# Kernel tuning notes

Hardware: AMD Instinct MI355X
Metric: run time of the kernel (lower is better)

## Reference

```python
import jax, jax.numpy as jnp
import numpy as np

B, N, D = 8, 1024, 1024
H, HD = 16, 64          # n_heads, head_dim = D // H
FF = 2 * D              # SwiGLU hidden dim (ffn_dim_mult=2)
EPS = 1e-5


def setup_inputs() -> dict:
    key = jax.random.key(0)
    ks = jax.random.split(key, 10)
    s = 0.02
    return {
        "x": jax.random.normal(ks[0], (B, N, D), dtype=jnp.float32),
        "attn_norm_scale": jnp.ones((D,), jnp.float32),
        "ffn_norm_scale": jnp.ones((D,), jnp.float32),
        "wq": jax.random.normal(ks[1], (D, D), jnp.float32) * s,
        "bq": jnp.zeros((D,), jnp.float32),
        "wk": jax.random.normal(ks[2], (D, D), jnp.float32) * s,
        "bk": jnp.zeros((D,), jnp.float32),
        "wv": jax.random.normal(ks[3], (D, D), jnp.float32) * s,
        "bv": jnp.zeros((D,), jnp.float32),
        "wo": jax.random.normal(ks[4], (D, D), jnp.float32) * s,
        "bo": jnp.zeros((D,), jnp.float32),
        "w_uv": jax.random.normal(ks[5], (D, 2 * FF), jnp.float32) * s,
        "w_out": jax.random.normal(ks[6], (FF, D), jnp.float32) * s,
    }


def _rmsnorm(x, scale):
    xf = x.astype(jnp.float32)
    y = xf * jax.lax.rsqrt(jnp.mean(xf * xf, axis=-1, keepdims=True) + EPS)
    return scale * y.astype(x.dtype)


def reference(x, attn_norm_scale, ffn_norm_scale, wq, bq, wk, bk, wv, bv,
              wo, bo, w_uv, w_out):
    # FFT2D: fft over channel dim then token dim, keep real part
    x = jnp.fft.fft(jnp.fft.fft(x, axis=-1), axis=-2).real.astype(jnp.float32)

    # --- self attention with pre-RMSNorm and residual ---
    xn = _rmsnorm(x, attn_norm_scale)
    q = (xn @ wq + bq).reshape(B, N, H, HD)
    k = (xn @ wk + bk).reshape(B, N, H, HD)
    v = (xn @ wv + bv).reshape(B, N, H, HD)
    scores = jnp.einsum('bnhd,bmhd->bhnm', q, k) / np.sqrt(HD).astype(np.float32)
    attn = jax.nn.softmax(scores, axis=-1)
    o = jnp.einsum('bhnm,bmhd->bnhd', attn, v).reshape(B, N, D)
    x = (o @ wo + bo) + x

    # --- SwiGLU FFN with pre-RMSNorm and residual ---
    xn = _rmsnorm(x, ffn_norm_scale)
    uv = xn @ w_uv                      # [B, N, 2*FF]
    u, vg = uv[..., :FF], uv[..., FF:]
    x = (jax.nn.silu(u) * vg) @ w_out + x
    return x
```

## Files before the change

kernel.cpp:

```cpp
#include <hip/hip_runtime.h>
#include <stdint.h>

typedef unsigned short u16;
typedef __attribute__((ext_vector_type(8))) __bf16 bf16x8;
typedef __attribute__((ext_vector_type(4))) float f32x4;
typedef __attribute__((ext_vector_type(8))) u16 u16x8;

static __device__ __forceinline__ u16 f2bf(float f){
  uint32_t x = __builtin_bit_cast(uint32_t, f);
  x = (x + 0x7FFFu + ((x >> 16) & 1u)) >> 16;
  return (u16)x;
}
static __device__ __forceinline__ u16 f2bf_fast(float f){
  uint32_t x = __builtin_bit_cast(uint32_t, f);
  return (u16)((x + 0x8000u) >> 16);
}
static __device__ __forceinline__ float bf2f(u16 h){
  uint32_t x = ((uint32_t)h) << 16;
  return __builtin_bit_cast(float, x);
}
static __device__ __forceinline__ f32x4 mfma16(bf16x8 a, bf16x8 b, f32x4 c){
  return __builtin_amdgcn_mfma_f32_16x16x32_bf16(a, b, c, 0, 0, 0);
}
static __device__ __forceinline__ void gload16(const void* g, void* l){
  __builtin_amdgcn_global_load_lds(
      (const __attribute__((address_space(1))) void*)(uintptr_t)g,
      (__attribute__((address_space(3))) void*)(uint32_t)(uintptr_t)l,
      16, 0, 0);
}

__global__ __launch_bounds__(256) void k_prep(
    const float* __restrict__ x,  const float* __restrict__ wq,
    const float* __restrict__ wk, const float* __restrict__ wv,
    const float* __restrict__ wo, const float* __restrict__ wuv,
    const float* __restrict__ wout,
    const float* __restrict__ bq, const float* __restrict__ bk,
    const float* __restrict__ bv,
    u16* __restrict__ Cb, u16* __restrict__ Sb, u16* __restrict__ xbt,
    u16* __restrict__ wqkvt, u16* __restrict__ wot, u16* __restrict__ wuvt,
    u16* __restrict__ woutt, float* __restrict__ bqkv)
{
  int bid = blockIdx.x;
  int t = threadIdx.x;
  if (bid < 1024){
    int n = bid, m0 = t * 4;
    #pragma unroll
    for (int i = 0; i < 4; ++i){
      int m = m0 + i;
      int ph = (n * m) & 1023;
      float a = (float)ph * (1.0f / 512.0f);
      int idx = n * 1024 + m;
      Cb[idx] = f2bf(cospif(a)); Sb[idx] = f2bf(sinpif(a));
    }
    return;
  }
  bid -= 1024;
  if (bid >= 18432){
    int i = (bid - 18432) * 256 + t;
    bqkv[i] = i < 1024 ? bq[i] : (i < 2048 ? bk[i - 1024] : bv[i - 2048]);
    return;
  }
  __shared__ float tl[32][33];
  const float* in; u16* out; int Cc, R, bx, by;
  int64_t inOff = 0, outOff = 0;
  bool uvperm = false;
  if (bid < 8192){
    int z = bid >> 10, tile = bid & 1023;
    in = x; out = xbt; Cc = 1024; R = 1024;
    inOff = (int64_t)z << 20; outOff = (int64_t)z << 20;
    bx = tile & 31; by = tile >> 5;
  } else if (bid < 12288){
    int j = (bid - 8192) >> 10, tile = (bid - 8192) & 1023;
    const float* srcs[4] = {wq, wk, wv, wo};
    in = srcs[j]; Cc = 1024; R = 1024;
    if (j < 3){ out = wqkvt; outOff = (int64_t)j << 20; }
    else      { out = wot; }
    bx = tile & 31; by = tile >> 5;
  } else if (bid < 16384){
    int tile = bid - 12288;
    in = wuv; out = wuvt; Cc = 4096; R = 1024; uvperm = true;
    bx = tile & 127; by = tile >> 7;
  } else {
    int tile = bid - 16384;
    in = wout; out = woutt; Cc = 1024; R = 2048;
    bx = tile & 31; by = tile >> 5;
  }
  int tc = bx * 32, tr = by * 32;
  int lx = t & 31, ly = t >> 5;
  const float* ip = in + inOff;
  #pragma unroll
  for (int i = 0; i < 32; i += 8)
    tl[ly + i][lx] = ip[(int64_t)(tr + ly + i) * Cc + tc + lx];
  __syncthreads();
  if (uvperm){
    #pragma unroll
    for (int i = 0; i < 32; i += 8){
      int c = tc + ly + i;
      int pr = (c < 2048) ? ((c >> 4) * 32 + (c & 15))
                          : (((c - 2048) >> 4) * 32 + 16 + ((c - 2048) & 15));
      out[(int64_t)pr * 1024 + tr + lx] = f2bf(tl[lx][ly + i]);
    }
  } else {
    u16* op = out + outOff;
    #pragma unroll
    for (int i = 0; i < 32; i += 8)
      op[(int64_t)(tc + ly + i) * R + tr + lx] = f2bf(tl[lx][ly + i]);
  }
}

__global__ __launch_bounds__(256) void k_rmsnorm(const float* __restrict__ x,
                                                 const float* __restrict__ sc,
                                                 u16* __restrict__ out){
  int r = blockIdx.x;
  const float4* px = (const float4*)(x + (int64_t)r * 1024);
  float4 v = px[threadIdx.x];
  float ss = v.x*v.x + v.y*v.y + v.z*v.z + v.w*v.w;
  #pragma unroll
  for (int o = 1; o < 64; o <<= 1) ss += __shfl_xor(ss, o);
  __shared__ float red[4];
  if ((threadIdx.x & 63) == 0) red[threadIdx.x >> 6] = ss;
  __syncthreads();
  float tot = red[0] + red[1] + red[2] + red[3];
  float rs = rsqrtf(tot * (1.0f / 1024.0f) + 1e-5f);
  float4 s4 = ((const float4*)sc)[threadIdx.x];
  ushort4 ov;
  ov.x = f2bf(v.x * rs * s4.x); ov.y = f2bf(v.y * rs * s4.y);
  ov.z = f2bf(v.z * rs * s4.z); ov.w = f2bf(v.w * rs * s4.w);
  ((ushort4*)(out + (int64_t)r * 1024))[threadIdx.x] = ov;
}

__global__ __launch_bounds__(256) void k_fftfin(const u16* __restrict__ Uw,
                                                const float* __restrict__ sc,
                                                float* __restrict__ Y,
                                                u16* __restrict__ xn){
  int row = blockIdx.x;
  int b = row >> 10, k = row & 1023;
  int kp = (k <= 512) ? k : 1024 - k;
  float sm = (k <= 512) ? 1.0f : -1.0f;
  const u16* ub = Uw + (int64_t)b * 819200 + (int64_t)kp * 640;
  const u16* wb = ub + 640 * 640;
  int c0 = threadIdx.x * 4;
  float y[4];
  #pragma unroll
  for (int i = 0; i < 4; ++i){
    int c = c0 + i;
    int tp = (c <= 512) ? c : 1024 - c;
    float st = (c <= 512) ? sm : -sm;
    y[i] = bf2f(ub[tp]) - st * bf2f(wb[tp]);
  }
  float ss = y[0]*y[0] + y[1]*y[1] + y[2]*y[2] + y[3]*y[3];
  #pragma unroll
  for (int o = 1; o < 64; o <<= 1) ss += __shfl_xor(ss, o);
  __shared__ float red[4];
  if ((threadIdx.x & 63) == 0) red[threadIdx.x >> 6] = ss;
  __syncthreads();
  float tot = red[0] + red[1] + red[2] + red[3];
  float rs = rsqrtf(tot * (1.0f / 1024.0f) + 1e-5f);
  float4 s4 = ((const float4*)sc)[threadIdx.x];
  float4 yo; yo.x = y[0]; yo.y = y[1]; yo.z = y[2]; yo.w = y[3];
  ((float4*)(Y + (int64_t)row * 1024))[threadIdx.x] = yo;
  ushort4 ov;
  ov.x = f2bf(y[0] * rs * s4.x); ov.y = f2bf(y[1] * rs * s4.y);
  ov.z = f2bf(y[2] * rs * s4.z); ov.w = f2bf(y[3] * rs * s4.w);
  ((ushort4*)(xn + (int64_t)row * 1024))[threadIdx.x] = ov;
}

template<bool SILU, bool COLCHUNK>
__global__ __launch_bounds__(256, 4) void k_gemm4(
    const u16* __restrict__ A0, const u16* __restrict__ A1,
    const u16* __restrict__ B0, const u16* __restrict__ B1,
    void* Cout, const float* __restrict__ bias, const float* resid,
    int nkt, int rowSplit, int lda, int ldb, int ldc,
    int64_t aB, int64_t bB, int64_t cB, int outBf16)
{
  __shared__ char smem[32768];

  int z = blockIdx.z;
  int nwg = gridDim.x * gridDim.y;
  int bid = blockIdx.y * gridDim.x + blockIdx.x;
  int q = nwg >> 3, r = nwg & 7, xc = bid & 7, off = bid >> 3;
  int sw = (xc < r ? xc * (q + 1) : r * (q + 1) + (xc - r) * q) + off;
  int bx, by;
  if (COLCHUNK){ bx = sw / gridDim.y; by = sw % gridDim.y; }
  else         { bx = sw % gridDim.x; by = sw / gridDim.x; }

  int tm = by * 128, tn = bx * 128;
  int tid = threadIdx.x;
  int lane = tid & 63, w = tid >> 6;
  int lr = lane & 15, lg = lane >> 4;
  int wOffM = (w >> 1) * 64, wOffN = (w & 1) * 64;

  const u16* Ap = ((tm < rowSplit) ? A0 : A1) + (int64_t)z * aB;
  const u16* Bp = ((tm < rowSplit) ? B0 : B1) + (int64_t)z * bB;
  int64_t cOff = (int64_t)z * cB;

  int r0_, kg0_, r1_, kg1_;
  {
    int D = tid * 16, line = D >> 7, sp = ((D >> 4) & 7) ^ (line & 7);
    r0_ = line * 2 + (sp >> 2); kg0_ = sp & 3;
    D = tid * 16 + 4096; line = D >> 7; sp = ((D >> 4) & 7) ^ (line & 7);
    r1_ = line * 2 + (sp >> 2); kg1_ = sp & 3;
  }
  const u16* pA0 = Ap + (int64_t)(tm + r0_) * lda + kg0_ * 8;
  const u16* pA1 = Ap + (int64_t)(tm + r1_) * lda + kg1_ * 8;
  const u16* pB0 = Bp + (int64_t)(tn + r0_) * ldb + kg0_ * 8;
  const u16* pB1 = Bp + (int64_t)(tn + r1_) * ldb + kg1_ * 8;

  int slotR = (lg + ((lr & 1) << 2)) ^ ((lr >> 1) & 7);
  int aRB = ((wOffM >> 1) + (lr >> 1)) * 128 + slotR * 16;
  int bRB = ((wOffN >> 1) + (lr >> 1)) * 128 + slotR * 16;

  const f32x4 fz = {0.f, 0.f, 0.f, 0.f};
  f32x4 acc[4][4];
  #pragma unroll
  for (int i = 0; i < 4; ++i)
    #pragma unroll
    for (int j = 0; j < 4; ++j) acc[i][j] = fz;

  auto STAGE = [&](int kt, int bf){
    int k0 = kt * 32;
    char* d = smem + bf * 16384 + tid * 16;
    gload16(pA0 + k0, d);
    gload16(pA1 + k0, d + 4096);
    gload16(pB0 + k0, d + 8192);
    gload16(pB1 + k0, d + 12288);
  };
  auto COMPUTE = [&](const char* Ab){
    const char* Bb = Ab + 8192;
    bf16x8 af[4], bfr[4];
    #pragma unroll
    for (int i = 0; i < 4; ++i) af[i]  = *(const bf16x8*)(Ab + aRB + i * 1024);
    #pragma unroll
    for (int j = 0; j < 4; ++j) bfr[j] = *(const bf16x8*)(Bb + bRB + j * 1024);
    #pragma unroll
    for (int i = 0; i < 4; ++i)
      #pragma unroll
      for (int j = 0; j < 4; ++j)
        acc[i][j] = mfma16(af[i], bfr[j], acc[i][j]);
  };

  STAGE(0, 0);
  __syncthreads();
  for (int kt = 0; kt < nkt; kt += 2){
    STAGE(kt + 1, 1);
    COMPUTE(smem);
    __syncthreads();
    if (kt + 2 < nkt) STAGE(kt + 2, 0);
    COMPUTE(smem + 16384);
    __syncthreads();
  }

  if constexpr (SILU){
    int colBase = ((tn + wOffN) >> 1) + lr;
    #pragma unroll
    for (int i = 0; i < 4; ++i){
      #pragma unroll
      for (int jj = 0; jj < 4; ++jj){
        int row = tm + wOffM + i * 16 + lg * 4 + jj;
        #pragma unroll
        for (int jp = 0; jp < 2; ++jp){
          float u = acc[i][jp * 2][jj], v = acc[i][jp * 2 + 1][jj];
          float s = u / (1.0f + __expf(-u));
          ((u16*)Cout)[(int64_t)row * ldc + colBase + jp * 16] = f2bf(s * v);
        }
      }
    }
  } else {
    #pragma unroll
    for (int i = 0; i < 4; ++i){
      #pragma unroll
      for (int j = 0; j < 4; ++j){
        int col = tn + wOffN + j * 16 + lr;
        float badd = bias ? bias[col] : 0.0f;
        #pragma unroll
        for (int jj = 0; jj < 4; ++jj){
          int row = tm + wOffM + i * 16 + lg * 4 + jj;
          int64_t idx = cOff + (int64_t)row * ldc + col;
          float v = acc[i][j][jj] + badd;
          if (resid) v += resid[idx];
          if (outBf16) ((u16*)Cout)[idx] = f2bf(v);
          else         ((float*)Cout)[idx] = v;
        }
      }
    }
  }
}

__global__ __launch_bounds__(256) void k_vtrans(const u16* __restrict__ qkv,
                                                u16* __restrict__ vt){
  __shared__ u16 T[64 * 65];
  int bh = blockIdx.y; int b = bh >> 4, h = bh & 15;
  int kt = blockIdx.x;
  int t = threadIdx.x;
  const u16* src = qkv + (int64_t)(b * 1024 + kt * 64) * 3072 + 2048 + h * 64;
  #pragma unroll
  for (int i = 0; i < 16; ++i){
    int idx = i * 256 + t;
    int r = idx >> 6, c = idx & 63;
    T[r * 65 + c] = src[(int64_t)r * 3072 + c];
  }
  __syncthreads();
  u16* dst = vt + (int64_t)bh * 65536 + kt * 64;
  #pragma unroll
  for (int i = 0; i < 16; ++i){
    int idx = i * 256 + t;
    int dr = idx >> 6, kc = idx & 63;
    dst[(int64_t)dr * 1024 + kc] = T[kc * 65 + dr];
  }
}

__global__ __launch_bounds__(512, 4) void k_attn2(const u16* __restrict__ qkv,
                                                  const u16* __restrict__ vt,
                                                  u16* __restrict__ O){
  __shared__ u16 Ks[2][4096];
  __shared__ u16 Vts[2][4096];
  __shared__ u16 Pl[8][2304];
  int bh = blockIdx.y; int b = bh >> 4, h = bh & 15;
  int qt = blockIdx.x;
  int t = threadIdx.x, w = t >> 6, lane = t & 63, lr = lane & 15, lg = lane >> 4;
  int sr = t >> 3, sl = t & 7;
  int swz = (sl ^ (sr & 7)) * 8;

  const u16* kg = qkv + (int64_t)b * 1024 * 3072 + 1024 + h * 64;
  const u16* vg = vt + (int64_t)bh * 65536;

  const u16* qrow = qkv + (int64_t)(b * 1024 + qt * 256 + w * 32 + lr) * 3072 + h * 64;
  bf16x8 aq[2][2];
  #pragma unroll
  for (int m = 0; m < 2; ++m)
    #pragma unroll
    for (int kc = 0; kc < 2; ++kc)
      aq[m][kc] = *(const bf16x8*)(qrow + (int64_t)m * 16 * 3072 + kc * 32 + lg * 8);

  const f32x4 fz = {0.f, 0.f, 0.f, 0.f};
  f32x4 o_[2][4];
  float lj[2][4];
  #pragma unroll
  for (int m = 0; m < 2; ++m){
    #pragma unroll
    for (int d = 0; d < 4; ++d) o_[m][d] = fz;
    #pragma unroll
    for (int j = 0; j < 4; ++j) lj[m][j] = 0.f;
  }

  #define STAGE(ktile, bn) do {                                                   \
    gload16(kg + (int64_t)((ktile) * 64 + sr) * 3072 + swz,                       \
            (char*)Ks + (bn) * 8192 + t * 16);                                    \
    gload16(vg + (int64_t)sr * 1024 + (ktile) * 64 + swz,                         \
            (char*)Vts + (bn) * 8192 + t * 16);                                   \
  } while (0)

  STAGE(0, 0);
  __syncthreads();
  int buf = 0;
  int lsw = lr & 7;

  const float CSC = 0.1803368801111204f;
  const float MSH = 8.656170245333781f;

  #pragma unroll 1
  for (int kt = 0; kt < 16; ++kt){
    if (kt < 15) STAGE(kt + 1, buf ^ 1);

    f32x4 s[2][4];
    #pragma unroll
    for (int m = 0; m < 2; ++m)
      #pragma unroll
      for (int n = 0; n < 4; ++n) s[m][n] = fz;
    #pragma unroll
    for (int n = 0; n < 4; ++n){
      #pragma unroll
      for (int kc = 0; kc < 2; ++kc){
        bf16x8 kb = *(const bf16x8*)&Ks[buf][(n * 16 + lr) * 64 + (((kc * 4 + lg) ^ lsw) * 8)];
        s[0][n] = mfma16(aq[0][kc], kb, s[0][n]);
        s[1][n] = mfma16(aq[1][kc], kb, s[1][n]);
      }
    }

    #pragma unroll
    for (int m = 0; m < 2; ++m){
      #pragma unroll
      for (int j = 0; j < 4; ++j){
        float p0 = exp2f(fmaf(s[m][0][j], CSC, -MSH));
        float p1 = exp2f(fmaf(s[m][1][j], CSC, -MSH));
        float p2 = exp2f(fmaf(s[m][2][j], CSC, -MSH));
        float p3 = exp2f(fmaf(s[m][3][j], CSC, -MSH));
        lj[m][j] += (p0 + p1) + (p2 + p3);
        u16* pb = &Pl[w][(m * 16 + lg * 4 + j) * 72 + lr];
        pb[0]  = f2bf_fast(p0); pb[16] = f2bf_fast(p1);
        pb[32] = f2bf_fast(p2); pb[48] = f2bf_fast(p3);
      }
    }
    asm volatile("s_waitcnt lgkmcnt(0)" ::: "memory");
    __builtin_amdgcn_sched_barrier(0);

    #pragma unroll
    for (int kc = 0; kc < 2; ++kc){
      bf16x8 pa0 = *(const bf16x8*)&Pl[w][(lr) * 72 + kc * 32 + lg * 8];
      bf16x8 pa1 = *(const bf16x8*)&Pl[w][(16 + lr) * 72 + kc * 32 + lg * 8];
      #pragma unroll
      for (int dt = 0; dt < 4; ++dt){
        bf16x8 vb = *(const bf16x8*)&Vts[buf][(dt * 16 + lr) * 64 + (((kc * 4 + lg) ^ lsw) * 8)];
        o_[0][dt] = mfma16(pa0, vb, o_[0][dt]);
        o_[1][dt] = mfma16(pa1, vb, o_[1][dt]);
      }
    }
    __syncthreads();
    buf ^= 1;
  }
  #undef STAGE

  u16* obase = O + (int64_t)(b * 1024 + qt * 256 + w * 32) * 1024 + h * 64;
  #pragma unroll
  for (int m = 0; m < 2; ++m){
    #pragma unroll
    for (int j = 0; j < 4; ++j){
      float l = lj[m][j];
      l += __shfl_xor(l, 1); l += __shfl_xor(l, 2);
      l += __shfl_xor(l, 4); l += __shfl_xor(l, 8);
      float inv = 1.0f / l;
      int q = m * 16 + lg * 4 + j;
      #pragma unroll
      for (int dt = 0; dt < 4; ++dt)
        obase[(int64_t)q * 1024 + dt * 16 + lr] = f2bf(o_[m][dt][j] * inv);
    }
  }
}

extern "C" void kernel_launch(void* const* d_in, const int* in_sizes, int n_in,
                              void* d_out, int out_size, void* d_ws, size_t ws_size,
                              hipStream_t stream)
{
  (void)in_sizes; (void)n_in; (void)out_size; (void)ws_size;
  const float* x    = (const float*)d_in[0];
  const float* ans  = (const float*)d_in[1];
  const float* fns  = (const float*)d_in[2];
  const float* wq   = (const float*)d_in[3];
  const float* bq   = (const float*)d_in[4];
  const float* wk   = (const float*)d_in[5];
  const float* bk   = (const float*)d_in[6];
  const float* wv   = (const float*)d_in[7];
  const float* bvv  = (const float*)d_in[8];
  const float* wo   = (const float*)d_in[9];
  const float* bo   = (const float*)d_in[10];
  const float* wuv  = (const float*)d_in[11];
  const float* wout = (const float*)d_in[12];

  char* ws = (char*)d_ws;
  const size_t MB = 1u << 20;
  const int64_t M1 = 1024 * 1024;
  const int64_t FB = (int64_t)1280 * 1024;
  const int64_t FB2 = (int64_t)1280 * 640;
  const int BIG = 1 << 30;
  u16*  xbt   = (u16*)(ws + 0 * MB);
  u16*  Xcs   = (u16*)(ws + 16 * MB);
  u16*  Uw    = (u16*)(ws + 36 * MB);
  u16*  xn    = (u16*)(ws + 56 * MB);
  u16*  qkv   = (u16*)(ws + 0 * MB);
  u16*  vtg   = (u16*)(ws + 72 * MB);
  u16*  Obuf  = (u16*)(ws + 88 * MB);
  u16*  xn2   = (u16*)(ws + 0 * MB);
  u16*  g     = (u16*)(ws + 16 * MB);
  u16*  Cb    = (u16*)(ws + 104 * MB);
  u16*  Sb    = (u16*)(ws + 106 * MB);
  u16*  wqkvt = (u16*)(ws + 108 * MB);
  u16*  wot   = (u16*)(ws + 114 * MB);
  u16*  wuvt  = (u16*)(ws + 116 * MB);
  u16*  woutt = (u16*)(ws + 124 * MB);
  float* bqkv = (float*)(ws + 128 * MB);
  float* outF = (float*)d_out;

  k_prep<<<dim3(19468), 256, 0, stream>>>(x, wq, wk, wv, wo, wuv, wout,
      bq, bk, bvv, Cb, Sb, xbt, wqkvt, wot, wuvt, woutt, bqkv);

  k_gemm4<false, true><<<dim3(8, 10, 8), 256, 0, stream>>>(
      Cb, Sb - 640 * 1024, xbt, xbt, Xcs, nullptr, nullptr,
      32, 640, 1024, 1024, 1024, 0, M1, FB, 1);
  k_gemm4<false, false><<<dim3(5, 10, 8), 256, 0, stream>>>(
      Xcs, Xcs, Cb, Sb, Uw, nullptr, nullptr,
      32, 640, 1024, 1024, 640, FB, 0, FB2, 1);
  k_fftfin<<<dim3(8192), 256, 0, stream>>>(Uw, ans, outF, xn);

  k_gemm4<false, false><<<dim3(24, 64, 1), 256, 0, stream>>>(
      xn, xn, wqkvt, wqkvt, qkv, bqkv, nullptr,
      32, BIG, 1024, 1024, 3072, 0, 0, 0, 1);
  k_vtrans<<<dim3(16, 128), 256, 0, stream>>>(qkv, vtg);
  k_attn2<<<dim3(4, 128), 512, 0, stream>>>(qkv, vtg, Obuf);
  k_gemm4<false, false><<<dim3(8, 64, 1), 256, 0, stream>>>(
      Obuf, Obuf, wot, wot, d_out, bo, outF,
      32, BIG, 1024, 1024, 1024, 0, 0, 0, 0);

  k_rmsnorm<<<dim3(8192), 256, 0, stream>>>(outF, fns, xn2);
  k_gemm4<true, false><<<dim3(32, 64, 1), 256, 0, stream>>>(
      xn2, xn2, wuvt, wuvt, g, nullptr, nullptr,
      32, BIG, 1024, 1024, 2048, 0, 0, 0, 1);
  k_gemm4<false, false><<<dim3(8, 64, 1), 256, 0, stream>>>(
      g, g, woutt, woutt, d_out, nullptr, outF,
      64, BIG, 2048, 2048, 1024, 0, 0, 0, 0);
}
```

Measured before the change: 411.4 us.

## Fuse V transpose into QKV GEMM epilogue and group tile rasterization

The QKV projection GEMM now writes the V columns directly in transposed per-head layout into the vt buffer, which removes the separate k_vtrans kernel and its extra global read and write of V. The non-column-chunk GEMMs also switch to a grouped tile ordering of width 16 or 8 columns to improve L2 reuse of the B operand. In exchange, the V part of the QKV output is no longer written to the row-major qkv buffer, and the transposed stores are strided across rows of 1024.

```diff
diff --git a/kernel.cpp b/kernel.cpp
--- a/kernel.cpp
+++ b/kernel.cpp
@@ -170,6 +170,7 @@
     const u16* __restrict__ A0, const u16* __restrict__ A1,
     const u16* __restrict__ B0, const u16* __restrict__ B1,
     void* Cout, const float* __restrict__ bias, const float* resid,
+    u16* __restrict__ vtbuf, int vtn0,
     int nkt, int rowSplit, int lda, int ldb, int ldc,
     int64_t aB, int64_t bB, int64_t cB, int outBf16)
 {
@@ -181,8 +182,16 @@
   int q = nwg >> 3, r = nwg & 7, xc = bid & 7, off = bid >> 3;
   int sw = (xc < r ? xc * (q + 1) : r * (q + 1) + (xc - r) * q) + off;
   int bx, by;
-  if (COLCHUNK){ bx = sw / gridDim.y; by = sw % gridDim.y; }
-  else         { bx = sw % gridDim.x; by = sw / gridDim.x; }
+  if (COLCHUNK){
+    bx = sw / gridDim.y; by = sw % gridDim.y;
+  } else {
+    int gx = gridDim.x;
+    int GW = ((gx & 15) == 0) ? 16 : (((gx & 7) == 0) ? 8 : gx);
+    int gsz = GW * gridDim.y;
+    int grp = sw / gsz, rem = sw % gsz;
+    bx = grp * GW + rem % GW;
+    by = rem / GW;
+  }
 
   int tm = by * 128, tn = bx * 128;
   int tid = threadIdx.x;
@@ -265,47 +274,45 @@
         }
       }
     }
-  } else {
-    #pragma unroll
-    for (int i = 0; i < 4; ++i){
-      #pragma unroll
-      for (int j = 0; j < 4; ++j){
-        int col = tn + wOffN + j * 16 + lr;
-        float badd = bias ? bias[col] : 0.0f;
-        #pragma unroll
-        for (int jj = 0; jj < 4; ++jj){
-          int row = tm + wOffM + i * 16 + lg * 4 + jj;
-          int64_t idx = cOff + (int64_t)row * ldc + col;
-          float v = acc[i][j][jj] + badd;
-          if (resid) v += resid[idx];
-          if (outBf16) ((u16*)Cout)[idx] = f2bf(v);
-          else         ((float*)Cout)[idx] = v;
-        }
+    return;
+  }
+  if (vtbuf && tn >= vtn0){
+    int b = tm >> 10;
+    int key0 = (tm & 1023) + wOffM + lg * 4;
+    #pragma unroll
+    for (int j = 0; j < 4; ++j){
+      int col = tn + wOffN + j * 16 + lr;
+      int hv = (col - 2048) >> 6, d = (col - 2048) & 63;
+      float badd = bias ? bias[col] : 0.0f;
+      u16* vb = vtbuf + ((int64_t)(b * 16 + hv) << 16) + d * 1024;
+      #pragma unroll
+      for (int i = 0; i < 4; ++i){
+        ushort4 pk;
+        pk.x = f2bf(acc[i][j][0] + badd);
+        pk.y = f2bf(acc[i][j][1] + badd);
+        pk.z = f2bf(acc[i][j][2] + badd);
+        pk.w = f2bf(acc[i][j][3] + badd);
+        *(ushort4*)(vb + key0 + i * 16) = pk;
       }
     }
-  }
-}
-
-__global__ __launch_bounds__(256) void k_vtrans(const u16* __restrict__ qkv,
-                                                u16* __restrict__ vt){
-  __shared__ u16 T[64 * 65];
-  int bh = blockIdx.y; int b = bh >> 4, h = bh & 15;
-  int kt = blockIdx.x;
-  int t = threadIdx.x;
-  const u16* src = qkv + (int64_t)(b * 1024 + kt * 64) * 3072 + 2048 + h * 64;
-  #pragma unroll
-  for (int i = 0; i < 16; ++i){
-    int idx = i * 256 + t;
-    int r = idx >> 6, c = idx & 63;
-    T[r * 65 + c] = src[(int64_t)r * 3072 + c];
-  }
-  __syncthreads();
-  u16* dst = vt + (int64_t)bh * 65536 + kt * 64;
-  #pragma unroll
-  for (int i = 0; i < 16; ++i){
-    int idx = i * 256 + t;
-    int dr = idx >> 6, kc = idx & 63;
-    dst[(int64_t)dr * 1024 + kc] = T[kc * 65 + dr];
+    return;
+  }
+  #pragma unroll
+  for (int i = 0; i < 4; ++i){
+    #pragma unroll
+    for (int j = 0; j < 4; ++j){
+      int col = tn + wOffN + j * 16 + lr;
+      float badd = bias ? bias[col] : 0.0f;
+      #pragma unroll
+      for (int jj = 0; jj < 4; ++jj){
+        int row = tm + wOffM + i * 16 + lg * 4 + jj;
+        int64_t idx = cOff + (int64_t)row * ldc + col;
+        float v = acc[i][j][jj] + badd;
+        if (resid) v += resid[idx];
+        if (outBf16) ((u16*)Cout)[idx] = f2bf(v);
+        else         ((float*)Cout)[idx] = v;
+      }
+    }
   }
 }
 
@@ -474,27 +481,26 @@
       bq, bk, bvv, Cb, Sb, xbt, wqkvt, wot, wuvt, woutt, bqkv);
 
   k_gemm4<false, true><<<dim3(8, 10, 8), 256, 0, stream>>>(
-      Cb, Sb - 640 * 1024, xbt, xbt, Xcs, nullptr, nullptr,
+      Cb, Sb - 640 * 1024, xbt, xbt, Xcs, nullptr, nullptr, nullptr, BIG,
       32, 640, 1024, 1024, 1024, 0, M1, FB, 1);
   k_gemm4<false, false><<<dim3(5, 10, 8), 256, 0, stream>>>(
-      Xcs, Xcs, Cb, Sb, Uw, nullptr, nullptr,
+      Xcs, Xcs, Cb, Sb, Uw, nullptr, nullptr, nullptr, BIG,
       32, 640, 1024, 1024, 640, FB, 0, FB2, 1);
   k_fftfin<<<dim3(8192), 256, 0, stream>>>(Uw, ans, outF, xn);
 
   k_gemm4<false, false><<<dim3(24, 64, 1), 256, 0, stream>>>(
-      xn, xn, wqkvt, wqkvt, qkv, bqkv, nullptr,
+      xn, xn, wqkvt, wqkvt, qkv, bqkv, nullptr, vtg, 2048,
       32, BIG, 1024, 1024, 3072, 0, 0, 0, 1);
-  k_vtrans<<<dim3(16, 128), 256, 0, stream>>>(qkv, vtg);
   k_attn2<<<dim3(4, 128), 512, 0, stream>>>(qkv, vtg, Obuf);
   k_gemm4<false, false><<<dim3(8, 64, 1), 256, 0, stream>>>(
-      Obuf, Obuf, wot, wot, d_out, bo, outF,
+      Obuf, Obuf, wot, wot, d_out, bo, outF, nullptr, BIG,
       32, BIG, 1024, 1024, 1024, 0, 0, 0, 0);
 
   k_rmsnorm<<<dim3(8192), 256, 0, stream>>>(outF, fns, xn2);
   k_gemm4<true, false><<<dim3(32, 64, 1), 256, 0, stream>>>(
-      xn2, xn2, wuvt, wuvt, g, nullptr, nullptr,
+      xn2, xn2, wuvt, wuvt, g, nullptr, nullptr, nullptr, BIG,
       32, BIG, 1024, 1024, 2048, 0, 0, 0, 1);
   k_gemm4<false, false><<<dim3(8, 64, 1), 256, 0, stream>>>(
-      g, g, woutt, woutt, d_out, nullptr, outF,
+      g, g, woutt, woutt, d_out, nullptr, outF, nullptr, BIG,
       64, BIG, 2048, 2048, 1024, 0, 0, 0, 0);
 }
```

New measurement: 403.9 us (median of 2 runs). Within noise of the previous version (-1.8%).
